# Performance work log

Hardware: AMD Instinct MI355X
Metric: run time of the kernel (lower is better)

## Reference

```python
import jax, jax.numpy as jnp
import numpy as np

LN_EPS = 1e-5
BN_EPS = 1e-5


def setup_inputs() -> dict:
    key = jax.random.key(0)
    k0, k1, k2, k3 = jax.random.split(key, 4)
    N, C, T, V, S = 128, 64, 128, 25, 3  # batch, channels, frames, joints, subsets
    rel = C // 8                          # rel_channels = 8
    inner = rel * S                       # hidden_dim * n_heads = 24
    x = jax.random.normal(k0, (N, C, T, V), dtype=jnp.float32)
    # graph adjacency parameter (3 subsets over 25 joints); small positive values
    PA = jax.random.uniform(k1, (S, V, V), dtype=jnp.float32) * 0.1
    ln_gamma = jnp.ones((C,), jnp.float32)
    ln_beta = jnp.zeros((C,), jnp.float32)
    # to_qk: Linear(C, 2*inner), weight init normal(0, 1) per source
    Wqk = jax.random.normal(k2, (2 * inner, C), dtype=jnp.float32)
    bqk = jnp.zeros((2 * inner,), jnp.float32)
    # conv_branch_init: normal(0, sqrt(2/(out*1*1*branches)))
    conv_w = jax.random.normal(k3, (S, C, C), dtype=jnp.float32) * np.float32(np.sqrt(2.0 / (C * S)))
    conv_b = jnp.zeros((S, C), jnp.float32)
    bn_gamma = jnp.ones((C,), jnp.float32)
    bn_beta = jnp.zeros((C,), jnp.float32)
    bn_mean = jnp.zeros((C,), jnp.float32)
    bn_var = jnp.ones((C,), jnp.float32)
    return {"x": x, "PA": PA, "ln_gamma": ln_gamma, "ln_beta": ln_beta,
            "Wqk": Wqk, "bqk": bqk, "conv_w": conv_w, "conv_b": conv_b,
            "bn_gamma": bn_gamma, "bn_beta": bn_beta, "bn_mean": bn_mean, "bn_var": bn_var}


def reference(x, PA, ln_gamma, ln_beta, Wqk, bqk, conv_w, conv_b,
              bn_gamma, bn_beta, bn_mean, bn_var):
    N, C, T, V = x.shape
    S = PA.shape[0]                       # num_subset == n_heads
    rel = Wqk.shape[0] // (2 * S)         # hidden dim per head
    scale = rel ** (-0.5)

    xv = jnp.transpose(x, (0, 2, 3, 1))   # n t v c

    # --- SelfAttention: LayerNorm -> Linear -> per-head softmax(q k^T) ---
    mu = jnp.mean(xv, axis=-1, keepdims=True)
    var = jnp.mean(jnp.square(xv - mu), axis=-1, keepdims=True)
    yn = (xv - mu) * jax.lax.rsqrt(var + LN_EPS) * ln_gamma + ln_beta
    qk = yn @ Wqk.T + bqk                 # n t v (2*inner)
    inner = qk.shape[-1] // 2
    q = qk[..., :inner].reshape(N, T, V, S, rel)
    k = qk[..., inner:].reshape(N, T, V, S, rel)
    dots = jnp.einsum('ntihd,ntjhd->nthij', q, k) * scale  # (n,t,h,V,V)
    attn = jax.nn.softmax(dots, axis=-1)

    # --- attention-modulated adjacency + per-subset aggregation ---
    A = attn * PA[None, None]             # (n,t,h,V,V)
    z = jnp.einsum('nthij,ntjc->nthic', A, xv)  # (n,t,h,V,C) messages per subset
    # per-subset 1x1 conv then sum over subsets
    out = jnp.einsum('nthvc,hoc->notv', z, conv_w) \
        + jnp.sum(conv_b, axis=0)[None, :, None, None]  # (n,C,t,V)

    # --- BatchNorm2d (eval-mode with provided stats) + residual + ReLU ---
    bn_out = (out - bn_mean[None, :, None, None]) \
        * jax.lax.rsqrt(bn_var + BN_EPS)[None, :, None, None] \
        * bn_gamma[None, :, None, None] + bn_beta[None, :, None, None]
    return jax.nn.relu(bn_out + x)        # down is identity since in_c == out_c
```

## Files before the change

kernel.cpp:

```cpp
#include <hip/hip_runtime.h>
#include <hip/hip_bf16.h>
#include <math.h>

typedef __attribute__((ext_vector_type(8))) short bf16x8;
typedef __attribute__((ext_vector_type(4))) float f32x4;

__device__ inline unsigned short f2bf(float f) {
    return __builtin_bit_cast(unsigned short, __float2bfloat16(f));
}
__device__ inline float bf2f(unsigned short u) {
    return __bfloat162float(__builtin_bit_cast(__hip_bfloat16, u));
}
__device__ inline bf16x8 cvt8(float4 a, float4 b) {
    bf16x8 r;
    r[0]=(short)f2bf(a.x); r[1]=(short)f2bf(a.y); r[2]=(short)f2bf(a.z); r[3]=(short)f2bf(a.w);
    r[4]=(short)f2bf(b.x); r[5]=(short)f2bf(b.y); r[6]=(short)f2bf(b.z); r[7]=(short)f2bf(b.w);
    return r;
}
__device__ inline void split8(float4 a, float4 b, bf16x8& hi, bf16x8& lo) {
    float f[8] = {a.x,a.y,a.z,a.w,b.x,b.y,b.z,b.w};
    #pragma unroll
    for (int i = 0; i < 8; ++i) {
        unsigned short h = f2bf(f[i]);
        hi[i] = (short)h;
        lo[i] = (short)f2bf(f[i] - bf2f(h));
    }
}

#define LDS_FLOATS 6403

__global__ __launch_bounds__(256, 6)
void agcn_fused_kernel(const float* __restrict__ x,
                       const float* __restrict__ PA,
                       const float* __restrict__ ln_g, const float* __restrict__ ln_b,
                       const float* __restrict__ Wqk, const float* __restrict__ bqk,
                       const float* __restrict__ conv_w, const float* __restrict__ conv_b,
                       const float* __restrict__ bn_g, const float* __restrict__ bn_b,
                       const float* __restrict__ bn_m, const float* __restrict__ bn_v,
                       float* __restrict__ out)
{
    __shared__ float lds[LDS_FLOATS];
    float* xv = lds;
    unsigned short* ynh = (unsigned short*)(lds + 1628);
    unsigned short* ynl = (unsigned short*)(lds + 2428);
    unsigned short* A_bf = (unsigned short*)(lds + 1628);
    float* qkb  = lds + 3228;
    unsigned short* xvT = (unsigned short*)(lds + 3228);
    float* Abuf = lds + 4528;
    unsigned short* zA  = (unsigned short*)(lds + 1628);
    float* res  = lds + 4528;

    const int bid = blockIdx.x;
    const int sid = ((bid & 7) << 11) | (bid >> 3);
    const int n = sid >> 7, t = sid & 127;
    const int tid = threadIdx.x;
    const int lane = tid & 63, w = tid >> 6;
    const int g = lane >> 4, l15 = lane & 15;

    const int o = 16 * w + l15;
    float4 cw_f[12];
    #pragma unroll
    for (int kt = 0; kt < 6; ++kt) {
        const float* wp = &conv_w[(kt >> 1) * 4096 + o * 64 + (kt & 1) * 32 + 8 * g];
        cw_f[2*kt]   = *(const float4*)wp;
        cw_f[2*kt+1] = *(const float4*)(wp + 4);
    }
    float4 wq_f[4];
    float bq = 0.f;
    if (w < 3) {
        const int j = 16 * w + l15;
        #pragma unroll
        for (int ks = 0; ks < 2; ++ks) {
            const float* wp = &Wqk[j * 64 + ks * 32 + 8 * g];
            wq_f[2*ks]   = *(const float4*)wp;
            wq_f[2*ks+1] = *(const float4*)(wp + 4);
        }
        bq = bqk[j];
    }

    const float* xbase = x + (size_t)n * 204800 + t * 25;
    for (int idx = tid; idx < 1600; idx += 256) {
        int c = idx / 25, v = idx - c * 25;
        xv[v * 65 + c] = xbase[c * 3200 + v];
    }

    bf16x8 cw[6];
    #pragma unroll
    for (int kt = 0; kt < 6; ++kt) cw[kt] = cvt8(cw_f[2*kt], cw_f[2*kt+1]);
    bf16x8 wqh[2], wql[2];
    if (w < 3) {
        #pragma unroll
        for (int ks = 0; ks < 2; ++ks) split8(wq_f[2*ks], wq_f[2*ks+1], wqh[ks], wql[ks]);
    }
    __syncthreads();

    {
        float lg = ln_g[lane], lb = ln_b[lane];
        for (int v = w; v < 25; v += 4) {
            float val = xv[v * 65 + lane];
            float s = val;
            for (int off = 32; off; off >>= 1) s += __shfl_xor(s, off);
            float mu = s * (1.0f / 64.0f);
            float d = val - mu;
            float s2 = d * d;
            for (int off = 32; off; off >>= 1) s2 += __shfl_xor(s2, off);
            float rstd = rsqrtf(s2 * (1.0f / 64.0f) + 1e-5f);
            float y = d * rstd * lg + lb;
            unsigned short h = f2bf(y);
            unsigned short l = f2bf(y - bf2f(h));
            int idx = (v * 64 + lane) ^ ((v & 7) << 3);
            ynh[idx] = h;
            ynl[idx] = l;
        }
    }
    __syncthreads();

    if (w < 3) {
        const int j = 16 * w + l15;
        #pragma unroll
        for (int mt = 0; mt < 2; ++mt) {
            f32x4 acc = {bq, bq, bq, bq};
            #pragma unroll
            for (int ks = 0; ks < 2; ++ks) {
                int row = 16 * mt + l15;
                int idx = (row * 64 + ks * 32 + 8 * g) ^ ((row & 7) << 3);
                bf16x8 ah = *(bf16x8*)&ynh[idx];
                bf16x8 al = *(bf16x8*)&ynl[idx];
                acc = __builtin_amdgcn_mfma_f32_16x16x32_bf16(al, wqh[ks], acc, 0, 0, 0);
                acc = __builtin_amdgcn_mfma_f32_16x16x32_bf16(ah, wql[ks], acc, 0, 0, 0);
                acc = __builtin_amdgcn_mfma_f32_16x16x32_bf16(ah, wqh[ks], acc, 0, 0, 0);
            }
            #pragma unroll
            for (int reg = 0; reg < 4; ++reg) {
                int v = 16 * mt + 4 * g + reg;
                if (v < 25) qkb[v * 52 + j] = acc[reg];
            }
        }
    }
    __syncthreads();

    for (int idx = tid; idx < 1875; idx += 256) {
        int h = idx / 625, r = idx - h * 625;
        int i = r / 25, j = r - i * 25;
        const float4* q = (const float4*)&qkb[i * 52 + h * 8];
        const float4* k = (const float4*)&qkb[j * 52 + 24 + h * 8];
        float4 q0 = q[0], q1 = q[1], k0 = k[0], k1 = k[1];
        float d = q0.x*k0.x + q0.y*k0.y + q0.z*k0.z + q0.w*k0.w
                + q1.x*k1.x + q1.y*k1.y + q1.z*k1.z + q1.w*k1.w;
        Abuf[idx] = d * 0.35355339059327373f;
    }
    __syncthreads();

    if (tid < 75) {
        int h = tid / 25, i = tid - h * 25;
        const float* row = &Abuf[h * 625 + i * 25];
        const float* pa = &PA[h * 625 + i * 25];
        float m = row[0];
        #pragma unroll
        for (int j = 1; j < 25; ++j) m = fmaxf(m, row[j]);
        float e[25];
        float s = 0.f;
        #pragma unroll
        for (int j = 0; j < 25; ++j) { e[j] = __expf(row[j] - m); s += e[j]; }
        float inv = 1.0f / s;
        unsigned short* ar = &A_bf[(h * 25 + i) * 40];
        #pragma unroll
        for (int j = 0; j < 25; ++j) ar[j] = f2bf(e[j] * inv * pa[j]);
        #pragma unroll
        for (int j = 25; j < 32; ++j) ar[j] = 0;
    }
    for (int idx = tid; idx < 2560; idx += 256) {
        int c = idx / 40, j = idx - c * 40;
        float val = (j < 25) ? xv[j * 65 + c] : 0.f;
        xvT[idx] = f2bf(val);
    }
    __syncthreads();

    f32x4 zacc[5];
    {
        bf16x8 bfrag = *(bf16x8*)&xvT[(16 * w + l15) * 40 + 8 * g];
        #pragma unroll
        for (int mt = 0; mt < 5; ++mt) {
            bf16x8 afrag = *(bf16x8*)&A_bf[(16 * mt + l15) * 40 + 8 * g];
            f32x4 a = {0.f, 0.f, 0.f, 0.f};
            zacc[mt] = __builtin_amdgcn_mfma_f32_16x16x32_bf16(afrag, bfrag, a, 0, 0, 0);
        }
    }
    __syncthreads();

    #pragma unroll
    for (int mt = 0; mt < 5; ++mt) {
        #pragma unroll
        for (int reg = 0; reg < 4; ++reg) {
            int r = 16 * mt + 4 * g + reg;
            if (r < 75) {
                int h = r / 25, i = r - h * 25;
                zA[i * 200 + h * 64 + 16 * w + l15] = f2bf(zacc[mt][reg]);
            }
        }
    }
    __syncthreads();

    {
        float bg = bn_g[o], bv = bn_v[o], bb = bn_b[o], bm = bn_m[o];
        float cb = conv_b[o] + conv_b[64 + o] + conv_b[128 + o];

        const int r1 = (16 + l15 < 25) ? (16 + l15) : 0;
        f32x4 acc0 = {0.f, 0.f, 0.f, 0.f}, acc1 = {0.f, 0.f, 0.f, 0.f};
        #pragma unroll
        for (int kt = 0; kt < 6; ++kt) {
            bf16x8 a0 = *(bf16x8*)&zA[l15 * 200 + 32 * kt + 8 * g];
            bf16x8 a1 = *(bf16x8*)&zA[r1 * 200 + 32 * kt + 8 * g];
            acc0 = __builtin_amdgcn_mfma_f32_16x16x32_bf16(a0, cw[kt], acc0, 0, 0, 0);
            acc1 = __builtin_amdgcn_mfma_f32_16x16x32_bf16(a1, cw[kt], acc1, 0, 0, 0);
        }
        float sc = bg * rsqrtf(bv + 1e-5f);
        float bi = cb * sc + bb - bm * sc;
        #pragma unroll
        for (int reg = 0; reg < 4; ++reg) {
            int v = 4 * g + reg;
            float val = acc0[reg] * sc + bi + xv[v * 65 + o];
            res[o * 25 + v] = fmaxf(val, 0.f);
        }
        #pragma unroll
        for (int reg = 0; reg < 4; ++reg) {
            int v = 16 + 4 * g + reg;
            if (v < 25) {
                float val = acc1[reg] * sc + bi + xv[v * 65 + o];
                res[o * 25 + v] = fmaxf(val, 0.f);
            }
        }
    }
    __syncthreads();

    {
        float* ob = out + (size_t)n * 204800 + t * 25;
        for (int idx = tid; idx < 1600; idx += 256) {
            int c = idx / 25, v = idx - c * 25;
            ob[c * 3200 + v] = res[idx];
        }
    }
}

extern "C" void kernel_launch(void* const* d_in, const int* in_sizes, int n_in,
                              void* d_out, int out_size, void* d_ws, size_t ws_size,
                              hipStream_t stream) {
    const float* x      = (const float*)d_in[0];
    const float* PA     = (const float*)d_in[1];
    const float* ln_g   = (const float*)d_in[2];
    const float* ln_b   = (const float*)d_in[3];
    const float* Wqk    = (const float*)d_in[4];
    const float* bqk    = (const float*)d_in[5];
    const float* conv_w = (const float*)d_in[6];
    const float* conv_b = (const float*)d_in[7];
    const float* bn_g   = (const float*)d_in[8];
    const float* bn_b   = (const float*)d_in[9];
    const float* bn_m   = (const float*)d_in[10];
    const float* bn_v   = (const float*)d_in[11];
    float* outp = (float*)d_out;

    agcn_fused_kernel<<<dim3(128 * 128), dim3(256), 0, stream>>>(
        x, PA, ln_g, ln_b, Wqk, bqk, conv_w, conv_b,
        bn_g, bn_b, bn_m, bn_v, outp);
}
```

Measured before the change: 248.0 us.

## Compute attention logits and softmax with MFMA and register-level shuffles

Replaces the scalar q·k dot-product loop and the 75-thread serial softmax with split-bf16 MFMA tiles per head, followed by a wave-shuffle softmax done in registers. PA is preloaded into registers, and the xvT transpose moves onto the otherwise idle fourth wave so it overlaps the QK projection. The LDS layout is reworked, so LDS use grows and launch bounds drop from 6 to 4 blocks per CU. The swizzled block-to-(n,t) mapping is also removed. This cuts a sync stage and the serial softmax tail, at the cost of lower occupancy.

```diff
diff --git a/kernel.cpp b/kernel.cpp
--- a/kernel.cpp
+++ b/kernel.cpp
@@ -27,9 +27,9 @@
     }
 }
 
-#define LDS_FLOATS 6403
-
-__global__ __launch_bounds__(256, 6)
+#define LDS_FLOATS 7408
+
+__global__ __launch_bounds__(256, 4)
 void agcn_fused_kernel(const float* __restrict__ x,
                        const float* __restrict__ PA,
                        const float* __restrict__ ln_g, const float* __restrict__ ln_b,
@@ -41,18 +41,17 @@
 {
     __shared__ float lds[LDS_FLOATS];
     float* xv = lds;
-    unsigned short* ynh = (unsigned short*)(lds + 1628);
-    unsigned short* ynl = (unsigned short*)(lds + 2428);
-    unsigned short* A_bf = (unsigned short*)(lds + 1628);
-    float* qkb  = lds + 3228;
-    unsigned short* xvT = (unsigned short*)(lds + 3228);
-    float* Abuf = lds + 4528;
-    unsigned short* zA  = (unsigned short*)(lds + 1628);
-    float* res  = lds + 4528;
+    unsigned short* ynh  = (unsigned short*)(lds + 1628);
+    unsigned short* ynl  = (unsigned short*)(lds + 2428);
+    float* res = lds + 1628;
+    unsigned short* qk_h = (unsigned short*)(lds + 3228);
+    unsigned short* qk_l = (unsigned short*)(lds + 3928);
+    unsigned short* A_bf = (unsigned short*)(lds + 4628);
+    unsigned short* zA   = (unsigned short*)(lds + 4628);
+    unsigned short* xvT  = (unsigned short*)(lds + 6128);
 
     const int bid = blockIdx.x;
-    const int sid = ((bid & 7) << 11) | (bid >> 3);
-    const int n = sid >> 7, t = sid & 127;
+    const int n = bid >> 7, t = bid & 127;
     const int tid = threadIdx.x;
     const int lane = tid & 63, w = tid >> 6;
     const int g = lane >> 4, l15 = lane & 15;
@@ -67,6 +66,7 @@
     }
     float4 wq_f[4];
     float bq = 0.f;
+    f32x4 pa[2][2] = {{{0,0,0,0},{0,0,0,0}},{{0,0,0,0},{0,0,0,0}}};
     if (w < 3) {
         const int j = 16 * w + l15;
         #pragma unroll
@@ -76,6 +76,16 @@
             wq_f[2*ks+1] = *(const float4*)(wp + 4);
         }
         bq = bqk[j];
+        #pragma unroll
+        for (int mt = 0; mt < 2; ++mt)
+            #pragma unroll
+            for (int jt = 0; jt < 2; ++jt)
+                #pragma unroll
+                for (int reg = 0; reg < 4; ++reg) {
+                    int ii = 16*mt + 4*g + reg, jj = 16*jt + l15;
+                    if (ii < 25 && jj < 25)
+                        pa[mt][jt][reg] = PA[w * 625 + ii * 25 + jj];
+                }
     }
 
     const float* xbase = x + (size_t)n * 204800 + t * 25;
@@ -106,11 +116,11 @@
             for (int off = 32; off; off >>= 1) s2 += __shfl_xor(s2, off);
             float rstd = rsqrtf(s2 * (1.0f / 64.0f) + 1e-5f);
             float y = d * rstd * lg + lb;
-            unsigned short h = f2bf(y);
-            unsigned short l = f2bf(y - bf2f(h));
+            unsigned short hh = f2bf(y);
+            unsigned short ll = f2bf(y - bf2f(hh));
             int idx = (v * 64 + lane) ^ ((v & 7) << 3);
-            ynh[idx] = h;
-            ynl[idx] = l;
+            ynh[idx] = hh;
+            ynl[idx] = ll;
         }
     }
     __syncthreads();
@@ -133,46 +143,82 @@
             #pragma unroll
             for (int reg = 0; reg < 4; ++reg) {
                 int v = 16 * mt + 4 * g + reg;
-                if (v < 25) qkb[v * 52 + j] = acc[reg];
-            }
-        }
-    }
-    __syncthreads();
-
-    for (int idx = tid; idx < 1875; idx += 256) {
-        int h = idx / 625, r = idx - h * 625;
-        int i = r / 25, j = r - i * 25;
-        const float4* q = (const float4*)&qkb[i * 52 + h * 8];
-        const float4* k = (const float4*)&qkb[j * 52 + 24 + h * 8];
-        float4 q0 = q[0], q1 = q[1], k0 = k[0], k1 = k[1];
-        float d = q0.x*k0.x + q0.y*k0.y + q0.z*k0.z + q0.w*k0.w
-                + q1.x*k1.x + q1.y*k1.y + q1.z*k1.z + q1.w*k1.w;
-        Abuf[idx] = d * 0.35355339059327373f;
-    }
-    __syncthreads();
-
-    if (tid < 75) {
-        int h = tid / 25, i = tid - h * 25;
-        const float* row = &Abuf[h * 625 + i * 25];
-        const float* pa = &PA[h * 625 + i * 25];
-        float m = row[0];
-        #pragma unroll
-        for (int j = 1; j < 25; ++j) m = fmaxf(m, row[j]);
-        float e[25];
-        float s = 0.f;
-        #pragma unroll
-        for (int j = 0; j < 25; ++j) { e[j] = __expf(row[j] - m); s += e[j]; }
-        float inv = 1.0f / s;
-        unsigned short* ar = &A_bf[(h * 25 + i) * 40];
-        #pragma unroll
-        for (int j = 0; j < 25; ++j) ar[j] = f2bf(e[j] * inv * pa[j]);
-        #pragma unroll
-        for (int j = 25; j < 32; ++j) ar[j] = 0;
-    }
-    for (int idx = tid; idx < 2560; idx += 256) {
-        int c = idx / 40, j = idx - c * 40;
-        float val = (j < 25) ? xv[j * 65 + c] : 0.f;
-        xvT[idx] = f2bf(val);
+                if (v < 25) {
+                    float q = acc[reg];
+                    unsigned short hh = f2bf(q);
+                    qk_h[v * 56 + j] = hh;
+                    qk_l[v * 56 + j] = f2bf(q - bf2f(hh));
+                }
+            }
+        }
+    } else {
+        for (int idx = lane; idx < 2560; idx += 64) {
+            int c = idx / 40, jj = idx - c * 40;
+            xvT[idx] = f2bf(jj < 25 ? xv[jj * 65 + c] : 0.f);
+        }
+    }
+    __syncthreads();
+
+    if (w < 3) {
+        const int h = w;
+        const bf16x8 zz = {0,0,0,0,0,0,0,0};
+        bf16x8 qhf[2], qlf[2], khf[2], klf[2];
+        #pragma unroll
+        for (int mt = 0; mt < 2; ++mt) {
+            int row = 16 * mt + l15;
+            bf16x8 a = *(bf16x8*)&qk_h[row * 56 + 8 * h];
+            bf16x8 b = *(bf16x8*)&qk_l[row * 56 + 8 * h];
+            qhf[mt] = (g == 0) ? a : zz;
+            qlf[mt] = (g == 0) ? b : zz;
+        }
+        #pragma unroll
+        for (int jt = 0; jt < 2; ++jt) {
+            int row = 16 * jt + l15;
+            bf16x8 a = *(bf16x8*)&qk_h[row * 56 + 24 + 8 * h];
+            bf16x8 b = *(bf16x8*)&qk_l[row * 56 + 24 + 8 * h];
+            khf[jt] = (g == 0) ? a : zz;
+            klf[jt] = (g == 0) ? b : zz;
+        }
+        f32x4 dacc[2][2];
+        #pragma unroll
+        for (int mt = 0; mt < 2; ++mt)
+            #pragma unroll
+            for (int jt = 0; jt < 2; ++jt) {
+                f32x4 a = {0.f, 0.f, 0.f, 0.f};
+                a = __builtin_amdgcn_mfma_f32_16x16x32_bf16(qlf[mt], khf[jt], a, 0, 0, 0);
+                a = __builtin_amdgcn_mfma_f32_16x16x32_bf16(qhf[mt], klf[jt], a, 0, 0, 0);
+                a = __builtin_amdgcn_mfma_f32_16x16x32_bf16(qhf[mt], khf[jt], a, 0, 0, 0);
+                dacc[mt][jt] = a;
+            }
+        const float SC = 0.35355339059327373f;
+        #pragma unroll
+        for (int mt = 0; mt < 2; ++mt) {
+            #pragma unroll
+            for (int reg = 0; reg < 4; ++reg) {
+                float v0 = dacc[mt][0][reg] * SC;
+                float v1 = dacc[mt][1][reg] * SC;
+                float m = fmaxf(v0, (l15 < 9) ? v1 : -3.0e38f);
+                m = fmaxf(m, __shfl_xor(m, 1));
+                m = fmaxf(m, __shfl_xor(m, 2));
+                m = fmaxf(m, __shfl_xor(m, 4));
+                m = fmaxf(m, __shfl_xor(m, 8));
+                float e0 = __expf(v0 - m);
+                float e1 = (l15 < 9) ? __expf(v1 - m) : 0.f;
+                float s = e0 + e1;
+                s += __shfl_xor(s, 1);
+                s += __shfl_xor(s, 2);
+                s += __shfl_xor(s, 4);
+                s += __shfl_xor(s, 8);
+                float inv = 1.0f / s;
+                int i = 16 * mt + 4 * g + reg;
+                if (i < 25) {
+                    unsigned short* rp = &A_bf[(h * 25 + i) * 40];
+                    rp[l15] = f2bf(e0 * inv * pa[mt][0][reg]);
+                    rp[16 + l15] = (l15 < 9) ? f2bf(e1 * inv * pa[mt][1][reg])
+                                             : (unsigned short)0;
+                }
+            }
+        }
     }
     __syncthreads();
 
```

After: 318.6 us. 1.28x slower.

## Process four frames per block with register prefetch of next frame's input

Applied to the files above, without the earlier changes.

Each block now handles four consecutive time frames instead of one, which amortizes the per-block loads and bf16 conversion of conv and qk weights and the BN constant setup. The next frame's x slice is loaded into registers while the current frame is being computed, then written to LDS after the output store. The xvT transpose is moved to threads idle during softmax. The cost is a 4x smaller grid with less parallelism and longer serial blocks, more registers for the prefetch buffer, and the removal of the previous block-index swizzle.

```diff
diff --git a/kernel.cpp b/kernel.cpp
--- a/kernel.cpp
+++ b/kernel.cpp
@@ -41,23 +41,23 @@
 {
     __shared__ float lds[LDS_FLOATS];
     float* xv = lds;
-    unsigned short* ynh = (unsigned short*)(lds + 1628);
-    unsigned short* ynl = (unsigned short*)(lds + 2428);
+    unsigned short* ynh  = (unsigned short*)(lds + 1628);
+    unsigned short* ynl  = (unsigned short*)(lds + 2428);
     unsigned short* A_bf = (unsigned short*)(lds + 1628);
+    unsigned short* zA   = (unsigned short*)(lds + 1628);
     float* qkb  = lds + 3228;
-    unsigned short* xvT = (unsigned short*)(lds + 3228);
+    unsigned short* xvT  = (unsigned short*)(lds + 3228);
     float* Abuf = lds + 4528;
-    unsigned short* zA  = (unsigned short*)(lds + 1628);
     float* res  = lds + 4528;
 
     const int bid = blockIdx.x;
-    const int sid = ((bid & 7) << 11) | (bid >> 3);
-    const int n = sid >> 7, t = sid & 127;
+    const int n = bid >> 5;
+    const int tb = (bid & 31) << 2;
     const int tid = threadIdx.x;
     const int lane = tid & 63, w = tid >> 6;
     const int g = lane >> 4, l15 = lane & 15;
-
     const int o = 16 * w + l15;
+
     float4 cw_f[12];
     #pragma unroll
     for (int kt = 0; kt < 6; ++kt) {
@@ -77,11 +77,17 @@
         }
         bq = bqk[j];
     }
-
-    const float* xbase = x + (size_t)n * 204800 + t * 25;
-    for (int idx = tid; idx < 1600; idx += 256) {
-        int c = idx / 25, v = idx - c * 25;
-        xv[v * 65 + c] = xbase[c * 3200 + v];
+    const float lg = ln_g[lane], lb = ln_b[lane];
+    const float sc_e = bn_g[o] * rsqrtf(bn_v[o] + 1e-5f);
+    const float bi_e = (conv_b[o] + conv_b[64 + o] + conv_b[128 + o]) * sc_e
+                       + bn_b[o] - bn_m[o] * sc_e;
+
+    {
+        const float* xb = x + (size_t)n * 204800 + tb * 25;
+        for (int idx = tid; idx < 1600; idx += 256) {
+            int c = idx / 25, v = idx - c * 25;
+            xv[v * 65 + c] = xb[c * 3200 + v];
+        }
     }
 
     bf16x8 cw[6];
@@ -94,151 +100,172 @@
     }
     __syncthreads();
 
-    {
-        float lg = ln_g[lane], lb = ln_b[lane];
+    float pf[7];
+    #pragma unroll 1
+    for (int s = 0; s < 4; ++s) {
+        const int t = tb + s;
+
+        if (s < 3) {
+            const float* xb = x + (size_t)n * 204800 + (t + 1) * 25;
+            #pragma unroll
+            for (int k = 0; k < 7; ++k) {
+                int idx = tid + (k << 8);
+                if (idx < 1600) {
+                    int c = idx / 25, v = idx - c * 25;
+                    pf[k] = xb[c * 3200 + v];
+                }
+            }
+        }
+
         for (int v = w; v < 25; v += 4) {
             float val = xv[v * 65 + lane];
-            float s = val;
-            for (int off = 32; off; off >>= 1) s += __shfl_xor(s, off);
-            float mu = s * (1.0f / 64.0f);
+            float sm = val;
+            for (int off = 32; off; off >>= 1) sm += __shfl_xor(sm, off);
+            float mu = sm * (1.0f / 64.0f);
             float d = val - mu;
             float s2 = d * d;
             for (int off = 32; off; off >>= 1) s2 += __shfl_xor(s2, off);
             float rstd = rsqrtf(s2 * (1.0f / 64.0f) + 1e-5f);
             float y = d * rstd * lg + lb;
-            unsigned short h = f2bf(y);
-            unsigned short l = f2bf(y - bf2f(h));
+            unsigned short hh = f2bf(y);
+            unsigned short ll = f2bf(y - bf2f(hh));
             int idx = (v * 64 + lane) ^ ((v & 7) << 3);
-            ynh[idx] = h;
-            ynl[idx] = l;
-        }
-    }
-    __syncthreads();
-
-    if (w < 3) {
-        const int j = 16 * w + l15;
-        #pragma unroll
-        for (int mt = 0; mt < 2; ++mt) {
-            f32x4 acc = {bq, bq, bq, bq};
-            #pragma unroll
-            for (int ks = 0; ks < 2; ++ks) {
-                int row = 16 * mt + l15;
-                int idx = (row * 64 + ks * 32 + 8 * g) ^ ((row & 7) << 3);
-                bf16x8 ah = *(bf16x8*)&ynh[idx];
-                bf16x8 al = *(bf16x8*)&ynl[idx];
-                acc = __builtin_amdgcn_mfma_f32_16x16x32_bf16(al, wqh[ks], acc, 0, 0, 0);
-                acc = __builtin_amdgcn_mfma_f32_16x16x32_bf16(ah, wql[ks], acc, 0, 0, 0);
-                acc = __builtin_amdgcn_mfma_f32_16x16x32_bf16(ah, wqh[ks], acc, 0, 0, 0);
-            }
-            #pragma unroll
-            for (int reg = 0; reg < 4; ++reg) {
-                int v = 16 * mt + 4 * g + reg;
-                if (v < 25) qkb[v * 52 + j] = acc[reg];
-            }
-        }
-    }
-    __syncthreads();
-
-    for (int idx = tid; idx < 1875; idx += 256) {
-        int h = idx / 625, r = idx - h * 625;
-        int i = r / 25, j = r - i * 25;
-        const float4* q = (const float4*)&qkb[i * 52 + h * 8];
-        const float4* k = (const float4*)&qkb[j * 52 + 24 + h * 8];
-        float4 q0 = q[0], q1 = q[1], k0 = k[0], k1 = k[1];
-        float d = q0.x*k0.x + q0.y*k0.y + q0.z*k0.z + q0.w*k0.w
-                + q1.x*k1.x + q1.y*k1.y + q1.z*k1.z + q1.w*k1.w;
-        Abuf[idx] = d * 0.35355339059327373f;
-    }
-    __syncthreads();
-
-    if (tid < 75) {
-        int h = tid / 25, i = tid - h * 25;
-        const float* row = &Abuf[h * 625 + i * 25];
-        const float* pa = &PA[h * 625 + i * 25];
-        float m = row[0];
-        #pragma unroll
-        for (int j = 1; j < 25; ++j) m = fmaxf(m, row[j]);
-        float e[25];
-        float s = 0.f;
-        #pragma unroll
-        for (int j = 0; j < 25; ++j) { e[j] = __expf(row[j] - m); s += e[j]; }
-        float inv = 1.0f / s;
-        unsigned short* ar = &A_bf[(h * 25 + i) * 40];
-        #pragma unroll
-        for (int j = 0; j < 25; ++j) ar[j] = f2bf(e[j] * inv * pa[j]);
-        #pragma unroll
-        for (int j = 25; j < 32; ++j) ar[j] = 0;
-    }
-    for (int idx = tid; idx < 2560; idx += 256) {
-        int c = idx / 40, j = idx - c * 40;
-        float val = (j < 25) ? xv[j * 65 + c] : 0.f;
-        xvT[idx] = f2bf(val);
-    }
-    __syncthreads();
-
-    f32x4 zacc[5];
-    {
-        bf16x8 bfrag = *(bf16x8*)&xvT[(16 * w + l15) * 40 + 8 * g];
+            ynh[idx] = hh;
+            ynl[idx] = ll;
+        }
+        __syncthreads();
+
+        if (w < 3) {
+            const int j = 16 * w + l15;
+            #pragma unroll
+            for (int mt = 0; mt < 2; ++mt) {
+                f32x4 acc = {bq, bq, bq, bq};
+                #pragma unroll
+                for (int ks = 0; ks < 2; ++ks) {
+                    int row = 16 * mt + l15;
+                    int idx = (row * 64 + ks * 32 + 8 * g) ^ ((row & 7) << 3);
+                    bf16x8 ah = *(bf16x8*)&ynh[idx];
+                    bf16x8 al = *(bf16x8*)&ynl[idx];
+                    acc = __builtin_amdgcn_mfma_f32_16x16x32_bf16(al, wqh[ks], acc, 0, 0, 0);
+                    acc = __builtin_amdgcn_mfma_f32_16x16x32_bf16(ah, wql[ks], acc, 0, 0, 0);
+                    acc = __builtin_amdgcn_mfma_f32_16x16x32_bf16(ah, wqh[ks], acc, 0, 0, 0);
+                }
+                #pragma unroll
+                for (int reg = 0; reg < 4; ++reg) {
+                    int v = 16 * mt + 4 * g + reg;
+                    if (v < 25) qkb[v * 52 + j] = acc[reg];
+                }
+            }
+        }
+        __syncthreads();
+
+        for (int idx = tid; idx < 1875; idx += 256) {
+            int h = idx / 625, r = idx - h * 625;
+            int i = r / 25, j = r - i * 25;
+            const float4* q = (const float4*)&qkb[i * 52 + h * 8];
+            const float4* k = (const float4*)&qkb[j * 52 + 24 + h * 8];
+            float4 q0 = q[0], q1 = q[1], k0 = k[0], k1 = k[1];
+            float d = q0.x*k0.x + q0.y*k0.y + q0.z*k0.z + q0.w*k0.w
+                    + q1.x*k1.x + q1.y*k1.y + q1.z*k1.z + q1.w*k1.w;
+            Abuf[idx] = d * 0.35355339059327373f;
+        }
+        __syncthreads();
+
+        if (tid < 75) {
+            int h = tid / 25, i = tid - h * 25;
+            const float* row = &Abuf[h * 625 + i * 25];
+            const float* pa = &PA[h * 625 + i * 25];
+            float m = row[0];
+            #pragma unroll
+            for (int j = 1; j < 25; ++j) m = fmaxf(m, row[j]);
+            float e[25];
+            float sm = 0.f;
+            #pragma unroll
+            for (int j = 0; j < 25; ++j) { e[j] = __expf(row[j] - m); sm += e[j]; }
+            float inv = 1.0f / sm;
+            unsigned short* ar = &A_bf[(h * 25 + i) * 40];
+            #pragma unroll
+            for (int j = 0; j < 25; ++j) ar[j] = f2bf(e[j] * inv * pa[j]);
+            #pragma unroll
+            for (int j = 25; j < 32; ++j) ar[j] = 0;
+        } else if (tid >= 96) {
+            for (int idx = tid - 96; idx < 2560; idx += 160) {
+                int c = idx / 40, jj = idx - c * 40;
+                xvT[idx] = f2bf(jj < 25 ? xv[jj * 65 + c] : 0.f);
+            }
+        }
+        __syncthreads();
+
+        f32x4 zacc[5];
+        {
+            bf16x8 bfrag = *(bf16x8*)&xvT[(16 * w + l15) * 40 + 8 * g];
+            #pragma unroll
+            for (int mt = 0; mt < 5; ++mt) {
+                bf16x8 afrag = *(bf16x8*)&A_bf[(16 * mt + l15) * 40 + 8 * g];
+                f32x4 a = {0.f, 0.f, 0.f, 0.f};
+                zacc[mt] = __builtin_amdgcn_mfma_f32_16x16x32_bf16(afrag, bfrag, a, 0, 0, 0);
+            }
+        }
+        __syncthreads();
+
         #pragma unroll
         for (int mt = 0; mt < 5; ++mt) {
-            bf16x8 afrag = *(bf16x8*)&A_bf[(16 * mt + l15) * 40 + 8 * g];
-            f32x4 a = {0.f, 0.f, 0.f, 0.f};
-            zacc[mt] = __builtin_amdgcn_mfma_f32_16x16x32_bf16(afrag, bfrag, a, 0, 0, 0);
-        }
-    }
-    __syncthreads();
-
-    #pragma unroll
-    for (int mt = 0; mt < 5; ++mt) {
-        #pragma unroll
-        for (int reg = 0; reg < 4; ++reg) {
-            int r = 16 * mt + 4 * g + reg;
-            if (r < 75) {
-                int h = r / 25, i = r - h * 25;
-                zA[i * 200 + h * 64 + 16 * w + l15] = f2bf(zacc[mt][reg]);
-            }
-        }
-    }
-    __syncthreads();
-
-    {
-        float bg = bn_g[o], bv = bn_v[o], bb = bn_b[o], bm = bn_m[o];
-        float cb = conv_b[o] + conv_b[64 + o] + conv_b[128 + o];
-
-        const int r1 = (16 + l15 < 25) ? (16 + l15) : 0;
-        f32x4 acc0 = {0.f, 0.f, 0.f, 0.f}, acc1 = {0.f, 0.f, 0.f, 0.f};
-        #pragma unroll
-        for (int kt = 0; kt < 6; ++kt) {
-            bf16x8 a0 = *(bf16x8*)&zA[l15 * 200 + 32 * kt + 8 * g];
-            bf16x8 a1 = *(bf16x8*)&zA[r1 * 200 + 32 * kt + 8 * g];
-            acc0 = __builtin_amdgcn_mfma_f32_16x16x32_bf16(a0, cw[kt], acc0, 0, 0, 0);
-            acc1 = __builtin_amdgcn_mfma_f32_16x16x32_bf16(a1, cw[kt], acc1, 0, 0, 0);
-        }
-        float sc = bg * rsqrtf(bv + 1e-5f);
-        float bi = cb * sc + bb - bm * sc;
-        #pragma unroll
-        for (int reg = 0; reg < 4; ++reg) {
-            int v = 4 * g + reg;
-            float val = acc0[reg] * sc + bi + xv[v * 65 + o];
-            res[o * 25 + v] = fmaxf(val, 0.f);
-        }
-        #pragma unroll
-        for (int reg = 0; reg < 4; ++reg) {
-            int v = 16 + 4 * g + reg;
-            if (v < 25) {
-                float val = acc1[reg] * sc + bi + xv[v * 65 + o];
+            #pragma unroll
+            for (int reg = 0; reg < 4; ++reg) {
+                int r = 16 * mt + 4 * g + reg;
+                if (r < 75) {
+                    int h = r / 25, i = r - h * 25;
+                    zA[i * 200 + h * 64 + 16 * w + l15] = f2bf(zacc[mt][reg]);
+                }
+            }
+        }
+        __syncthreads();
+
+        {
+            const int r1 = (16 + l15 < 25) ? (16 + l15) : 0;
+            f32x4 acc0 = {0.f, 0.f, 0.f, 0.f}, acc1 = {0.f, 0.f, 0.f, 0.f};
+            #pragma unroll
+            for (int kt = 0; kt < 6; ++kt) {
+                bf16x8 a0 = *(bf16x8*)&zA[l15 * 200 + 32 * kt + 8 * g];
+                bf16x8 a1 = *(bf16x8*)&zA[r1 * 200 + 32 * kt + 8 * g];
+                acc0 = __builtin_amdgcn_mfma_f32_16x16x32_bf16(a0, cw[kt], acc0, 0, 0, 0);
+                acc1 = __builtin_amdgcn_mfma_f32_16x16x32_bf16(a1, cw[kt], acc1, 0, 0, 0);
+            }
+            #pragma unroll
+            for (int reg = 0; reg < 4; ++reg) {
+                int v = 4 * g + reg;
+                float val = acc0[reg] * sc_e + bi_e + xv[v * 65 + o];
                 res[o * 25 + v] = fmaxf(val, 0.f);
             }
-        }
-    }
-    __syncthreads();
-
-    {
-        float* ob = out + (size_t)n * 204800 + t * 25;
-        for (int idx = tid; idx < 1600; idx += 256) {
-            int c = idx / 25, v = idx - c * 25;
-            ob[c * 3200 + v] = res[idx];
-        }
+            #pragma unroll
+            for (int reg = 0; reg < 4; ++reg) {
+                int v = 16 + 4 * g + reg;
+                if (v < 25) {
+                    float val = acc1[reg] * sc_e + bi_e + xv[v * 65 + o];
+                    res[o * 25 + v] = fmaxf(val, 0.f);
+                }
+            }
+        }
+        __syncthreads();
+
+        {
+            float* ob = out + (size_t)n * 204800 + t * 25;
+            for (int idx = tid; idx < 1600; idx += 256) {
+                int c = idx / 25, v = idx - c * 25;
+                ob[c * 3200 + v] = res[idx];
+            }
+            if (s < 3) {
+                #pragma unroll
+                for (int k = 0; k < 7; ++k) {
+                    int idx = tid + (k << 8);
+                    if (idx < 1600) {
+                        int c = idx / 25, v = idx - c * 25;
+                        xv[v * 65 + c] = pf[k];
+                    }
+                }
+            }
+        }
+        __syncthreads();
     }
 }
 
@@ -259,7 +286,7 @@
     const float* bn_v   = (const float*)d_in[11];
     float* outp = (float*)d_out;
 
-    agcn_fused_kernel<<<dim3(128 * 128), dim3(256), 0, stream>>>(
+    agcn_fused_kernel<<<dim3(4096), dim3(256), 0, stream>>>(
         x, PA, ln_g, ln_b, Wqk, bqk, conv_w, conv_b,
         bn_g, bn_b, bn_m, bn_v, outp);
 }
```

New measurement: 429.3 us. 73.1% more time.

## Restructure LayerNorm, xvT transpose, and softmax phases with vectorized LDS access

Applied to the files above, without the earlier changes.

The LayerNorm now uses 8 lanes per joint with float4 loads from a row-padded (stride 68) xv buffer and one-pass sum/sumsq. It writes packed bf16x8 hi/lo values. The bf16 transposed xvT is built in the same phase, which removes a separate pass. Softmax is split across two threads per row with shuffle reductions, and the BN/LN parameter loads are hoisted to kernel start. The block index swizzle is dropped, and the LDS footprint grows, so launch bounds drop from 6 to 5 blocks per CU, which may reduce occupancy.

```diff
diff --git a/kernel.cpp b/kernel.cpp
--- a/kernel.cpp
+++ b/kernel.cpp
@@ -27,9 +27,9 @@
     }
 }
 
-#define LDS_FLOATS 6403
-
-__global__ __launch_bounds__(256, 6)
+#define LDS_FLOATS 7755
+
+__global__ __launch_bounds__(256, 5)
 void agcn_fused_kernel(const float* __restrict__ x,
                        const float* __restrict__ PA,
                        const float* __restrict__ ln_g, const float* __restrict__ ln_b,
@@ -41,23 +41,22 @@
 {
     __shared__ float lds[LDS_FLOATS];
     float* xv = lds;
-    unsigned short* ynh = (unsigned short*)(lds + 1628);
-    unsigned short* ynl = (unsigned short*)(lds + 2428);
-    unsigned short* A_bf = (unsigned short*)(lds + 1628);
-    float* qkb  = lds + 3228;
-    unsigned short* xvT = (unsigned short*)(lds + 3228);
-    float* Abuf = lds + 4528;
-    unsigned short* zA  = (unsigned short*)(lds + 1628);
-    float* res  = lds + 4528;
+    unsigned short* ynh  = (unsigned short*)(lds + 1700);
+    unsigned short* ynl  = (unsigned short*)(lds + 2500);
+    float* qkb  = lds + 3300;
+    unsigned short* xvT  = (unsigned short*)(lds + 4600);
+    float* Abuf = lds + 5880;
+    unsigned short* A_bf = (unsigned short*)(lds + 1700);
+    unsigned short* zA   = (unsigned short*)(lds + 1700);
+    float* res  = lds + 5880;
 
     const int bid = blockIdx.x;
-    const int sid = ((bid & 7) << 11) | (bid >> 3);
-    const int n = sid >> 7, t = sid & 127;
+    const int n = bid >> 7, t = bid & 127;
     const int tid = threadIdx.x;
     const int lane = tid & 63, w = tid >> 6;
     const int g = lane >> 4, l15 = lane & 15;
-
     const int o = 16 * w + l15;
+
     float4 cw_f[12];
     #pragma unroll
     for (int kt = 0; kt < 6; ++kt) {
@@ -77,11 +76,21 @@
         }
         bq = bqk[j];
     }
-
-    const float* xbase = x + (size_t)n * 204800 + t * 25;
-    for (int idx = tid; idx < 1600; idx += 256) {
-        int c = idx / 25, v = idx - c * 25;
-        xv[v * 65 + c] = xbase[c * 3200 + v];
+    const int c0 = (lane & 7) << 3;
+    const float4 lg0 = *(const float4*)&ln_g[c0];
+    const float4 lg1 = *(const float4*)&ln_g[c0 + 4];
+    const float4 lb0 = *(const float4*)&ln_b[c0];
+    const float4 lb1 = *(const float4*)&ln_b[c0 + 4];
+    const float sc_e = bn_g[o] * rsqrtf(bn_v[o] + 1e-5f);
+    const float bi_e = (conv_b[o] + conv_b[64 + o] + conv_b[128 + o]) * sc_e
+                       + bn_b[o] - bn_m[o] * sc_e;
+
+    {
+        const float* xb = x + (size_t)n * 204800 + t * 25;
+        for (int idx = tid; idx < 1600; idx += 256) {
+            int c = idx / 25, v = idx - c * 25;
+            xv[v * 68 + c] = xb[c * 3200 + v];
+        }
     }
 
     bf16x8 cw[6];
@@ -95,23 +104,42 @@
     __syncthreads();
 
     {
-        float lg = ln_g[lane], lb = ln_b[lane];
-        for (int v = w; v < 25; v += 4) {
-            float val = xv[v * 65 + lane];
-            float s = val;
-            for (int off = 32; off; off >>= 1) s += __shfl_xor(s, off);
-            float mu = s * (1.0f / 64.0f);
-            float d = val - mu;
-            float s2 = d * d;
-            for (int off = 32; off; off >>= 1) s2 += __shfl_xor(s2, off);
-            float rstd = rsqrtf(s2 * (1.0f / 64.0f) + 1e-5f);
-            float y = d * rstd * lg + lb;
-            unsigned short h = f2bf(y);
-            unsigned short l = f2bf(y - bf2f(h));
-            int idx = (v * 64 + lane) ^ ((v & 7) << 3);
-            ynh[idx] = h;
-            ynl[idx] = l;
-        }
+        const int v = (w << 3) + (lane >> 3);
+        if (v < 25) {
+            const float4* xp = (const float4*)&xv[v * 68 + c0];
+            float4 a = xp[0], b = xp[1];
+            float s1 = ((a.x + a.y) + (a.z + a.w)) + ((b.x + b.y) + (b.z + b.w));
+            float s2 = ((a.x*a.x + a.y*a.y) + (a.z*a.z + a.w*a.w))
+                     + ((b.x*b.x + b.y*b.y) + (b.z*b.z + b.w*b.w));
+            s1 += __shfl_xor(s1, 1);  s2 += __shfl_xor(s2, 1);
+            s1 += __shfl_xor(s1, 2);  s2 += __shfl_xor(s2, 2);
+            s1 += __shfl_xor(s1, 4);  s2 += __shfl_xor(s2, 4);
+            float mu = s1 * (1.0f / 64.0f);
+            float var = s2 * (1.0f / 64.0f) - mu * mu;
+            float rstd = rsqrtf(var + 1e-5f);
+            float xa[8] = {a.x,a.y,a.z,a.w,b.x,b.y,b.z,b.w};
+            float lg[8] = {lg0.x,lg0.y,lg0.z,lg0.w,lg1.x,lg1.y,lg1.z,lg1.w};
+            float lb[8] = {lb0.x,lb0.y,lb0.z,lb0.w,lb1.x,lb1.y,lb1.z,lb1.w};
+            bf16x8 hh8, ll8;
+            #pragma unroll
+            for (int i = 0; i < 8; ++i) {
+                float y = (xa[i] - mu) * rstd * lg[i] + lb[i];
+                unsigned short hh = f2bf(y);
+                hh8[i] = (short)hh;
+                ll8[i] = (short)f2bf(y - bf2f(hh));
+            }
+            int base = (v * 64 + c0) ^ ((v & 7) << 3);
+            *(bf16x8*)&ynh[base] = hh8;
+            *(bf16x8*)&ynl[base] = ll8;
+        }
+        int c = tid >> 2, j0 = (tid & 3) << 3;
+        bf16x8 pk;
+        #pragma unroll
+        for (int i = 0; i < 8; ++i) {
+            int j = j0 + i;
+            pk[i] = (j < 25) ? (short)f2bf(xv[j * 68 + c]) : (short)0;
+        }
+        *(bf16x8*)&xvT[c * 40 + j0] = pk;
     }
     __syncthreads();
 
@@ -143,36 +171,54 @@
         int h = idx / 625, r = idx - h * 625;
         int i = r / 25, j = r - i * 25;
         const float4* q = (const float4*)&qkb[i * 52 + h * 8];
-        const float4* k = (const float4*)&qkb[j * 52 + 24 + h * 8];
-        float4 q0 = q[0], q1 = q[1], k0 = k[0], k1 = k[1];
+        const float4* kp = (const float4*)&qkb[j * 52 + 24 + h * 8];
+        float4 q0 = q[0], q1 = q[1], k0 = kp[0], k1 = kp[1];
         float d = q0.x*k0.x + q0.y*k0.y + q0.z*k0.z + q0.w*k0.w
                 + q1.x*k1.x + q1.y*k1.y + q1.z*k1.z + q1.w*k1.w;
         Abuf[idx] = d * 0.35355339059327373f;
     }
     __syncthreads();
 
-    if (tid < 75) {
-        int h = tid / 25, i = tid - h * 25;
-        const float* row = &Abuf[h * 625 + i * 25];
+    if (tid < 150) {
+        int r = tid >> 1, hf = tid & 1;
+        int h = (r < 25) ? 0 : ((r < 50) ? 1 : 2);
+        int i = r - h * 25;
+        int j0 = hf ? 13 : 0;
+        const float* row = &Abuf[r * 25];
         const float* pa = &PA[h * 625 + i * 25];
-        float m = row[0];
-        #pragma unroll
-        for (int j = 1; j < 25; ++j) m = fmaxf(m, row[j]);
-        float e[25];
-        float s = 0.f;
-        #pragma unroll
-        for (int j = 0; j < 25; ++j) { e[j] = __expf(row[j] - m); s += e[j]; }
+        float rr[13];
+        #pragma unroll
+        for (int j = 0; j < 13; ++j) {
+            int jj = j0 + j;
+            rr[j] = (jj < 25) ? row[jj] : -3.0e38f;
+        }
+        float m0 = fmaxf(rr[0], rr[1]), m1 = fmaxf(rr[2], rr[3]);
+        float m2 = fmaxf(rr[4], rr[5]), m3 = fmaxf(rr[6], rr[7]);
+        float m4 = fmaxf(rr[8], rr[9]), m5 = fmaxf(rr[10], rr[11]);
+        float m = fmaxf(fmaxf(fmaxf(m0, m1), fmaxf(m2, m3)),
+                        fmaxf(fmaxf(m4, m5), rr[12]));
+        m = fmaxf(m, __shfl_xor(m, 1));
+        float e[13];
+        float s0 = 0.f, s1 = 0.f;
+        #pragma unroll
+        for (int j = 0; j < 12; j += 2) {
+            e[j]   = __expf(rr[j]   - m); s0 += e[j];
+            e[j+1] = __expf(rr[j+1] - m); s1 += e[j+1];
+        }
+        e[12] = __expf(rr[12] - m);
+        float s = (s0 + s1) + e[12];
+        s += __shfl_xor(s, 1);
         float inv = 1.0f / s;
-        unsigned short* ar = &A_bf[(h * 25 + i) * 40];
-        #pragma unroll
-        for (int j = 0; j < 25; ++j) ar[j] = f2bf(e[j] * inv * pa[j]);
-        #pragma unroll
-        for (int j = 25; j < 32; ++j) ar[j] = 0;
-    }
-    for (int idx = tid; idx < 2560; idx += 256) {
-        int c = idx / 40, j = idx - c * 40;
-        float val = (j < 25) ? xv[j * 65 + c] : 0.f;
-        xvT[idx] = f2bf(val);
+        unsigned short* ar = &A_bf[r * 40];
+        #pragma unroll
+        for (int j = 0; j < 13; ++j) {
+            int jj = j0 + j;
+            if (jj < 25) ar[jj] = f2bf(e[j] * inv * pa[jj]);
+        }
+        if (hf) {
+            #pragma unroll
+            for (int j = 25; j < 32; ++j) ar[j] = 0;
+        }
     }
     __syncthreads();
 
@@ -194,7 +240,8 @@
         for (int reg = 0; reg < 4; ++reg) {
             int r = 16 * mt + 4 * g + reg;
             if (r < 75) {
-                int h = r / 25, i = r - h * 25;
+                int h = (r < 25) ? 0 : ((r < 50) ? 1 : 2);
+                int i = r - h * 25;
                 zA[i * 200 + h * 64 + 16 * w + l15] = f2bf(zacc[mt][reg]);
             }
         }
@@ -202,9 +249,6 @@
     __syncthreads();
 
     {
-        float bg = bn_g[o], bv = bn_v[o], bb = bn_b[o], bm = bn_m[o];
-        float cb = conv_b[o] + conv_b[64 + o] + conv_b[128 + o];
-
         const int r1 = (16 + l15 < 25) ? (16 + l15) : 0;
         f32x4 acc0 = {0.f, 0.f, 0.f, 0.f}, acc1 = {0.f, 0.f, 0.f, 0.f};
         #pragma unroll
@@ -214,19 +258,17 @@
             acc0 = __builtin_amdgcn_mfma_f32_16x16x32_bf16(a0, cw[kt], acc0, 0, 0, 0);
             acc1 = __builtin_amdgcn_mfma_f32_16x16x32_bf16(a1, cw[kt], acc1, 0, 0, 0);
         }
-        float sc = bg * rsqrtf(bv + 1e-5f);
-        float bi = cb * sc + bb - bm * sc;
         #pragma unroll
         for (int reg = 0; reg < 4; ++reg) {
             int v = 4 * g + reg;
-            float val = acc0[reg] * sc + bi + xv[v * 65 + o];
+            float val = acc0[reg] * sc_e + bi_e + xv[v * 68 + o];
             res[o * 25 + v] = fmaxf(val, 0.f);
         }
         #pragma unroll
         for (int reg = 0; reg < 4; ++reg) {
             int v = 16 + 4 * g + reg;
             if (v < 25) {
-                float val = acc1[reg] * sc + bi + xv[v * 65 + o];
+                float val = acc1[reg] * sc_e + bi_e + xv[v * 68 + o];
                 res[o * 25 + v] = fmaxf(val, 0.f);
             }
         }
```

After: 270.8 us. +9.2%, slower.
